# Kernel optimization log

Hardware: AMD Instinct MI355X
Metric: run time of the kernel (lower is better)

Reference implementation:

```python
import jax, jax.numpy as jnp
import numpy as np

N_NODES = 100000
N_EDGES = 1600000
IN_FEATS = 256
OUT_FEATS = 128


def setup_inputs() -> dict:
    key = jax.random.key(0)
    k1, k2, k3, k4, k5 = jax.random.split(key, 5)
    feat = jax.random.normal(k1, (N_NODES, IN_FEATS), dtype=jnp.float32)
    # xavier_uniform-like init for the weight
    limit = float(np.sqrt(6.0 / (IN_FEATS + OUT_FEATS)))
    weight = jax.random.uniform(k2, (IN_FEATS, OUT_FEATS), dtype=jnp.float32,
                                minval=-limit, maxval=limit)
    edge_weight = jax.random.uniform(k3, (N_EDGES,), dtype=jnp.float32)
    src = jax.random.randint(k4, (N_EDGES,), 0, N_NODES, dtype=jnp.int64)
    dst = jax.random.randint(k5, (N_EDGES,), 0, N_NODES, dtype=jnp.int64)
    return {"feat": feat, "weight": weight, "edge_weight": edge_weight,
            "src": src, "dst": dst}


def reference(feat, weight, edge_weight, src, dst):
    N = feat.shape[0]
    ones = jnp.ones(src.shape, dtype=feat.dtype)
    # out/in degrees from edge list (clamped to >= 1), as in DGL
    out_deg = jnp.clip(jax.ops.segment_sum(ones, src, num_segments=N), 1.0)
    in_deg = jnp.clip(jax.ops.segment_sum(ones, dst, num_segments=N), 1.0)
    # norm == 'both': pre-scale sources by out_deg^-0.5
    feat_src = feat * (out_deg ** -0.5)[:, None]
    # in_feats > out_feats branch: transform (with tanh) BEFORE aggregation
    h = jnp.tanh(feat_src @ weight)                      # [N, out]
    # message = u_mul_e: h[src] * edge_weight, then sum per destination
    m = h[src] * edge_weight[:, None]                    # [E, out]
    rst = jax.ops.segment_sum(m, dst, num_segments=N)    # [N, out]
    # norm == 'both': post-scale by in_deg^-0.5
    rst = rst * (in_deg ** -0.5)[:, None]
    return rst
```

## Files before the change

kernel.cpp:

```cpp
#include <hip/hip_runtime.h>
#include <hip/hip_fp16.h>
#include <math.h>

#define N_NODES 100000
#define N_EDGES 1600000
#define IN_F 256
#define OUT_F 128
#define SCAN_TPB 256
#define SCAN_EPB 1024

#define HR 4
#define HRANGE 25000
#define HC 64
#define HCHUNK 25000
#define PWORDS (N_NODES / 2)

typedef _Float16 h8 __attribute__((ext_vector_type(8)));
typedef float f4 __attribute__((ext_vector_type(4)));

__global__ __launch_bounds__(256) void hist_kernel(
        const int* __restrict__ src, const int* __restrict__ dst,
        int* __restrict__ rank, unsigned int* __restrict__ partial_in,
        unsigned int* __restrict__ partial_out) {
    __shared__ unsigned int bins[HRANGE / 2];
    int b = blockIdx.x;
    int c = b >> 3;
    int tr = b & 7;
    int type = tr >> 2;
    int r = tr & 3;
    for (int i = threadIdx.x; i < HRANGE / 2; i += 256) bins[i] = 0;
    __syncthreads();
    const int* nodes = type ? src : dst;
    const int e0 = c * HCHUNK;
    const int lo = r * HRANGE;
    const int ngroups = HCHUNK / 4;
    for (int g = threadIdx.x; g < ngroups; g += 256) {
        int e = e0 + g * 4;
        int4 n4 = *(const int4*)(nodes + e);
        int nn[4] = {n4.x, n4.y, n4.z, n4.w};
        #pragma unroll
        for (int j = 0; j < 4; ++j) {
            unsigned loc = (unsigned)(nn[j] - lo);
            if (loc < (unsigned)HRANGE) {
                unsigned sh = (loc & 1) * 16;
                unsigned old = atomicAdd(&bins[loc >> 1], 1u << sh);
                if (type == 0) rank[e + j] = (int)((old >> sh) & 0xffffu);
            }
        }
    }
    __syncthreads();
    unsigned int* part = type ? partial_out : partial_in;
    unsigned int* dstp = part + (size_t)c * PWORDS + (lo >> 1);
    for (int i = threadIdx.x; i < HRANGE / 2; i += 256) dstp[i] = bins[i];
}

__global__ __launch_bounds__(256) void fused_reduce_kernel(
        const unsigned int* __restrict__ partial_in,
        const unsigned int* __restrict__ partial_out,
        unsigned short* __restrict__ chunk_base16,
        int* __restrict__ deg_in, float* __restrict__ rs_out,
        int* __restrict__ spart, int N) {
    __shared__ int tmp[256];
    int t = threadIdx.x;
    int n0 = blockIdx.x * SCAN_EPB + t * 4;
    int run[4] = {0, 0, 0, 0};
    int sout[4] = {0, 0, 0, 0};
    if (n0 < N) {
        const int w0 = n0 >> 1;
        #pragma unroll 4
        for (int c = 0; c < HC; ++c) {
            ushort4 cb;
            cb.x = (unsigned short)run[0]; cb.y = (unsigned short)run[1];
            cb.z = (unsigned short)run[2]; cb.w = (unsigned short)run[3];
            *(ushort4*)(chunk_base16 + (size_t)c * N_NODES + n0) = cb;
            uint2 pi = *(const uint2*)(partial_in + (size_t)c * PWORDS + w0);
            run[0] += (int)(pi.x & 0xffffu);  run[1] += (int)(pi.x >> 16);
            run[2] += (int)(pi.y & 0xffffu);  run[3] += (int)(pi.y >> 16);
            uint2 po = *(const uint2*)(partial_out + (size_t)c * PWORDS + w0);
            sout[0] += (int)(po.x & 0xffffu); sout[1] += (int)(po.x >> 16);
            sout[2] += (int)(po.y & 0xffffu); sout[3] += (int)(po.y >> 16);
        }
        *(int4*)(deg_in + n0) = make_int4(run[0], run[1], run[2], run[3]);
        float4 rs;
        rs.x = rsqrtf((float)(sout[0] < 1 ? 1 : sout[0]));
        rs.y = rsqrtf((float)(sout[1] < 1 ? 1 : sout[1]));
        rs.z = rsqrtf((float)(sout[2] < 1 ? 1 : sout[2]));
        rs.w = rsqrtf((float)(sout[3] < 1 ? 1 : sout[3]));
        *(float4*)(rs_out + n0) = rs;
    }
    tmp[t] = run[0] + run[1] + run[2] + run[3];
    __syncthreads();
    for (int off = 128; off > 0; off >>= 1) {
        if (t < off) tmp[t] += tmp[t + off];
        __syncthreads();
    }
    if (t == 0) spart[blockIdx.x] = tmp[0];
}

__global__ __launch_bounds__(128) void scan_part2(const int* __restrict__ partials,
                                                  int* __restrict__ bases, int nb) {
    __shared__ int tmp[128];
    int t = threadIdx.x;
    int v = (t < nb) ? partials[t] : 0;
    tmp[t] = v;
    __syncthreads();
    int x = v;
    for (int off = 1; off < 128; off <<= 1) {
        int y = (t >= off) ? tmp[t - off] : 0;
        __syncthreads();
        x += y;
        tmp[t] = x;
        __syncthreads();
    }
    if (t < nb) bases[t] = x - v;
}

__global__ __launch_bounds__(SCAN_TPB) void scan_part3(const int* __restrict__ deg,
                                                       const int* __restrict__ bases,
                                                       int* __restrict__ row_ptr, int N) {
    __shared__ int tmp[SCAN_TPB];
    int t = threadIdx.x;
    int i0 = blockIdx.x * SCAN_EPB + t * 4;
    int v[4];
    int s = 0;
    #pragma unroll
    for (int j = 0; j < 4; ++j) { v[j] = (i0 + j < N) ? deg[i0 + j] : 0; s += v[j]; }
    tmp[t] = s;
    __syncthreads();
    int x = s;
    for (int off = 1; off < SCAN_TPB; off <<= 1) {
        int y = (t >= off) ? tmp[t - off] : 0;
        __syncthreads();
        x += y;
        tmp[t] = x;
        __syncthreads();
    }
    int excl = bases[blockIdx.x] + x - s;
    #pragma unroll
    for (int j = 0; j < 4; ++j) {
        if (i0 + j < N) row_ptr[i0 + j] = excl;
        excl += v[j];
    }
    if (blockIdx.x == gridDim.x - 1 && t == SCAN_TPB - 1) row_ptr[N] = bases[blockIdx.x] + x;
}

__global__ __launch_bounds__(256) void fill_kernel(
        const int* __restrict__ src, const int* __restrict__ dst,
        const float* __restrict__ ew, const int* __restrict__ row_ptr,
        const unsigned short* __restrict__ chunk_base16,
        const int* __restrict__ rank, int2* __restrict__ ed, int E) {
    int e0 = (blockIdx.x * 256 + threadIdx.x) * 4;
    if (e0 >= E) return;
    int4 s4 = *(const int4*)(src + e0);
    int4 d4 = *(const int4*)(dst + e0);
    float4 w4 = *(const float4*)(ew + e0);
    int4 r4 = *(const int4*)(rank + e0);
    int c = e0 / HCHUNK;
    const unsigned short* cb = chunk_base16 + (size_t)c * N_NODES;
    int dd[4] = {d4.x, d4.y, d4.z, d4.w};
    int ss[4] = {s4.x, s4.y, s4.z, s4.w};
    int rr[4] = {r4.x, r4.y, r4.z, r4.w};
    float ww[4] = {w4.x, w4.y, w4.z, w4.w};
    #pragma unroll
    for (int j = 0; j < 4; ++j) {
        int d = dd[j];
        int p = row_ptr[d] + (int)cb[d] + rr[j];
        unsigned long long v = (unsigned long long)(unsigned int)ss[j] |
                               ((unsigned long long)(unsigned int)__float_as_int(ww[j]) << 32);
        __builtin_nontemporal_store(v, (unsigned long long*)&ed[p]);
    }
}

__global__ void wt_kernel(const float* __restrict__ W, _Float16* __restrict__ Wt) {
    int i = blockIdx.x * blockDim.x + threadIdx.x;
    if (i < IN_F * OUT_F) {
        int n = i >> 8;
        int k = i & 255;
        Wt[i] = (_Float16)W[k * OUT_F + n];
    }
}

__global__ __launch_bounds__(256) void gemm_mfma_kernel(
        const float* __restrict__ feat, const _Float16* __restrict__ Wt,
        const float* __restrict__ rs_out, __half* __restrict__ h, int N) {
    const int wave = threadIdx.x >> 6;
    const int lane = threadIdx.x & 63;
    const int m = lane & 15;
    const int quad = lane >> 4;
    const int rowbase = blockIdx.x * 64 + wave * 16;
    const int arow = rowbase + m;
    const bool rowok = arow < N;

    const float rs = rowok ? rs_out[arow] : 1.f;
    const float* ap = feat + (size_t)(rowok ? arow : 0) * IN_F + quad * 8;

    f4 acc[8];
    #pragma unroll
    for (int t = 0; t < 8; ++t) acc[t] = (f4){0.f, 0.f, 0.f, 0.f};

    #pragma unroll
    for (int k0 = 0; k0 < IN_F; k0 += 32) {
        float4 f0 = make_float4(0.f, 0.f, 0.f, 0.f);
        float4 f1 = make_float4(0.f, 0.f, 0.f, 0.f);
        if (rowok) {
            f0 = *(const float4*)(ap + k0);
            f1 = *(const float4*)(ap + k0 + 4);
        }
        h8 a;
        a[0] = (_Float16)(f0.x * rs); a[1] = (_Float16)(f0.y * rs);
        a[2] = (_Float16)(f0.z * rs); a[3] = (_Float16)(f0.w * rs);
        a[4] = (_Float16)(f1.x * rs); a[5] = (_Float16)(f1.y * rs);
        a[6] = (_Float16)(f1.z * rs); a[7] = (_Float16)(f1.w * rs);
        const int k = k0 + quad * 8;
        #pragma unroll
        for (int t = 0; t < 8; ++t) {
            h8 b = *(const h8*)&Wt[(size_t)(t * 16 + m) * IN_F + k];
            acc[t] = __builtin_amdgcn_mfma_f32_16x16x32_f16(a, b, acc[t], 0, 0, 0);
        }
    }

    const int crow0 = rowbase + quad * 4;
    #pragma unroll
    for (int t = 0; t < 8; ++t) {
        #pragma unroll
        for (int r = 0; r < 4; ++r) {
            int rr = crow0 + r;
            if (rr < N) h[(size_t)rr * OUT_F + t * 16 + m] = __float2half(tanhf(acc[t][r]));
        }
    }
}

__global__ __launch_bounds__(256) void gather_kernel(
        const __half* __restrict__ h, const int2* __restrict__ ed,
        const int* __restrict__ row_ptr, float* __restrict__ out, int N) {
    int wave = threadIdx.x >> 6;
    int lane = threadIdx.x & 63;
    int node = blockIdx.x * 4 + wave;
    if (node >= N) return;
    int lo = row_ptr[node];
    int hi = row_ptr[node + 1];
    int p = lane >> 4;
    int c = lane & 15;
    float acc[4][8];
    #pragma unroll
    for (int g = 0; g < 4; ++g)
        #pragma unroll
        for (int i = 0; i < 8; ++i) acc[g][i] = 0.f;

    for (int j = lo; j < hi; j += 16) {
        #pragma unroll
        for (int g = 0; g < 4; ++g) {
            int jj = j + g * 4 + p;
            int2 e = (jj < hi) ? ed[jj] : make_int2(0, 0);
            float w = __int_as_float(e.y);
            int4 rrow = *(const int4*)(h + (size_t)e.x * OUT_F + c * 8);
            float2 t;
            t = __half22float2(*(__half2*)&rrow.x); acc[g][0] += w * t.x; acc[g][1] += w * t.y;
            t = __half22float2(*(__half2*)&rrow.y); acc[g][2] += w * t.x; acc[g][3] += w * t.y;
            t = __half22float2(*(__half2*)&rrow.z); acc[g][4] += w * t.x; acc[g][5] += w * t.y;
            t = __half22float2(*(__half2*)&rrow.w); acc[g][6] += w * t.x; acc[g][7] += w * t.y;
        }
    }
    float v[8];
    #pragma unroll
    for (int i = 0; i < 8; ++i) {
        v[i] = (acc[0][i] + acc[1][i]) + (acc[2][i] + acc[3][i]);
        v[i] += __shfl_xor(v[i], 16);
        v[i] += __shfl_xor(v[i], 32);
    }
    if (p == 0) {
        int deg = hi - lo; if (deg < 1) deg = 1;
        float rs = rsqrtf((float)deg);
        float* op = out + (size_t)node * OUT_F + c * 8;
        *(float4*)op       = make_float4(v[0] * rs, v[1] * rs, v[2] * rs, v[3] * rs);
        *(float4*)(op + 4) = make_float4(v[4] * rs, v[5] * rs, v[6] * rs, v[7] * rs);
    }
}

extern "C" void kernel_launch(void* const* d_in, const int* in_sizes, int n_in,
                              void* d_out, int out_size, void* d_ws, size_t ws_size,
                              hipStream_t stream) {
    const float* feat   = (const float*)d_in[0];
    const float* weight = (const float*)d_in[1];
    const float* ew     = (const float*)d_in[2];
    const int*   src    = (const int*)d_in[3];
    const int*   dst    = (const int*)d_in[4];
    float* out = (float*)d_out;

    char* ws = (char*)d_ws;
    float* rs_out      = (float*)(ws);
    int*   deg_in      = (int*)(ws + 400000);
    int*   row_ptr     = (int*)(ws + 800000);
    int*   spart       = (int*)(ws + 1200016);
    int*   sbases      = (int*)(ws + 1200528);
    int*   rank        = (int*)(ws + 1201056);
    unsigned int* partial_in  = (unsigned int*)(ws + 7601056);
    int2*  ed          = (int2*)(ws + 7601056);
    unsigned short* chunk_base16 = (unsigned short*)(ws + 20401056);
    unsigned int* partial_out = (unsigned int*)(ws + 33201056);
    __half* h          = (__half*)(ws + 20401056);
    _Float16* Wt       = (_Float16*)(ws + 46001056);

    const int nb = (N_NODES + SCAN_EPB - 1) / SCAN_EPB;

    hist_kernel<<<2 * HR * HC, 256, 0, stream>>>(src, dst, rank, partial_in, partial_out);
    fused_reduce_kernel<<<nb, 256, 0, stream>>>(partial_in, partial_out, chunk_base16,
                                                deg_in, rs_out, spart, N_NODES);
    scan_part2<<<1, 128, 0, stream>>>(spart, sbases, nb);
    scan_part3<<<nb, SCAN_TPB, 0, stream>>>(deg_in, sbases, row_ptr, N_NODES);
    fill_kernel<<<(N_EDGES / 4 + 255) / 256, 256, 0, stream>>>(src, dst, ew, row_ptr,
                                                               chunk_base16, rank, ed, N_EDGES);
    wt_kernel<<<(IN_F * OUT_F + 255) / 256, 256, 0, stream>>>(weight, Wt);
    gemm_mfma_kernel<<<(N_NODES + 63) / 64, 256, 0, stream>>>(feat, Wt, rs_out, h, N_NODES);
    gather_kernel<<<(N_NODES + 3) / 4, 256, 0, stream>>>(h, ed, row_ptr, out, N_NODES);
}
```

Measured before the change: 412.9 us.

## Split GEMM by output columns per wave and keep weight fragments in registers

Each wave now owns 32 output columns and keeps its weight B-fragments in registers for the whole block. It loops over the block's 64 rows in pairs of 16-row tiles, rather than each wave owning 16 rows and reloading all of W for every k-step. The out-degree row scale moves from the fp32→fp16 input conversion to the accumulator epilogue, so each feature element needs one fewer multiply. The cost is that all four waves in a block now read the same feat rows, which leans on cache for reuse, and register pressure rises from holding 16 h8 B fragments.

Result: faster. 403.0 us (-2.4%).

```diff
diff --git a/kernel.cpp b/kernel.cpp
--- a/kernel.cpp
+++ b/kernel.cpp
@@ -187,45 +187,63 @@
     const int lane = threadIdx.x & 63;
     const int m = lane & 15;
     const int quad = lane >> 4;
-    const int rowbase = blockIdx.x * 64 + wave * 16;
-    const int arow = rowbase + m;
-    const bool rowok = arow < N;
-
-    const float rs = rowok ? rs_out[arow] : 1.f;
-    const float* ap = feat + (size_t)(rowok ? arow : 0) * IN_F + quad * 8;
-
-    f4 acc[8];
-    #pragma unroll
-    for (int t = 0; t < 8; ++t) acc[t] = (f4){0.f, 0.f, 0.f, 0.f};
-
-    #pragma unroll
-    for (int k0 = 0; k0 < IN_F; k0 += 32) {
-        float4 f0 = make_float4(0.f, 0.f, 0.f, 0.f);
-        float4 f1 = make_float4(0.f, 0.f, 0.f, 0.f);
-        if (rowok) {
-            f0 = *(const float4*)(ap + k0);
-            f1 = *(const float4*)(ap + k0 + 4);
-        }
-        h8 a;
-        a[0] = (_Float16)(f0.x * rs); a[1] = (_Float16)(f0.y * rs);
-        a[2] = (_Float16)(f0.z * rs); a[3] = (_Float16)(f0.w * rs);
-        a[4] = (_Float16)(f1.x * rs); a[5] = (_Float16)(f1.y * rs);
-        a[6] = (_Float16)(f1.z * rs); a[7] = (_Float16)(f1.w * rs);
-        const int k = k0 + quad * 8;
-        #pragma unroll
-        for (int t = 0; t < 8; ++t) {
-            h8 b = *(const h8*)&Wt[(size_t)(t * 16 + m) * IN_F + k];
-            acc[t] = __builtin_amdgcn_mfma_f32_16x16x32_f16(a, b, acc[t], 0, 0, 0);
-        }
-    }
-
-    const int crow0 = rowbase + quad * 4;
-    #pragma unroll
-    for (int t = 0; t < 8; ++t) {
-        #pragma unroll
-        for (int r = 0; r < 4; ++r) {
-            int rr = crow0 + r;
-            if (rr < N) h[(size_t)rr * OUT_F + t * 16 + m] = __float2half(tanhf(acc[t][r]));
+    const int n0 = wave * 32;
+
+    h8 b[2][8];
+    #pragma unroll
+    for (int t = 0; t < 2; ++t)
+        #pragma unroll
+        for (int k = 0; k < 8; ++k)
+            b[t][k] = *(const h8*)&Wt[(size_t)(n0 + t * 16 + m) * IN_F + k * 32 + quad * 8];
+
+    const int rowbase = blockIdx.x * 64;
+
+    #pragma unroll
+    for (int pair = 0; pair < 2; ++pair) {
+        const int r0 = rowbase + pair * 32;
+        int ar0 = r0 + m;       if (ar0 >= N) ar0 = 0;
+        int ar1 = r0 + 16 + m;  if (ar1 >= N) ar1 = 0;
+        const float* ap0 = feat + (size_t)ar0 * IN_F + quad * 8;
+        const float* ap1 = feat + (size_t)ar1 * IN_F + quad * 8;
+
+        f4 acc00 = {0.f, 0.f, 0.f, 0.f}, acc01 = {0.f, 0.f, 0.f, 0.f};
+        f4 acc10 = {0.f, 0.f, 0.f, 0.f}, acc11 = {0.f, 0.f, 0.f, 0.f};
+
+        #pragma unroll
+        for (int k = 0; k < 8; ++k) {
+            float4 f00 = *(const float4*)(ap0 + k * 32);
+            float4 f01 = *(const float4*)(ap0 + k * 32 + 4);
+            float4 f10 = *(const float4*)(ap1 + k * 32);
+            float4 f11 = *(const float4*)(ap1 + k * 32 + 4);
+            h8 a0, a1;
+            a0[0] = (_Float16)f00.x; a0[1] = (_Float16)f00.y;
+            a0[2] = (_Float16)f00.z; a0[3] = (_Float16)f00.w;
+            a0[4] = (_Float16)f01.x; a0[5] = (_Float16)f01.y;
+            a0[6] = (_Float16)f01.z; a0[7] = (_Float16)f01.w;
+            a1[0] = (_Float16)f10.x; a1[1] = (_Float16)f10.y;
+            a1[2] = (_Float16)f10.z; a1[3] = (_Float16)f10.w;
+            a1[4] = (_Float16)f11.x; a1[5] = (_Float16)f11.y;
+            a1[6] = (_Float16)f11.z; a1[7] = (_Float16)f11.w;
+            acc00 = __builtin_amdgcn_mfma_f32_16x16x32_f16(a0, b[0][k], acc00, 0, 0, 0);
+            acc01 = __builtin_amdgcn_mfma_f32_16x16x32_f16(a0, b[1][k], acc01, 0, 0, 0);
+            acc10 = __builtin_amdgcn_mfma_f32_16x16x32_f16(a1, b[0][k], acc10, 0, 0, 0);
+            acc11 = __builtin_amdgcn_mfma_f32_16x16x32_f16(a1, b[1][k], acc11, 0, 0, 0);
+        }
+
+        #pragma unroll
+        for (int tile = 0; tile < 2; ++tile) {
+            const f4 aL = tile ? acc10 : acc00;
+            const f4 aR = tile ? acc11 : acc01;
+            const int crow = r0 + tile * 16 + quad * 4;
+            #pragma unroll
+            for (int r = 0; r < 4; ++r) {
+                const int rr = crow + r;
+                if (rr < N) {
+                    const float rs = rs_out[rr];
+                    h[(size_t)rr * OUT_F + n0 + m]      = __float2half(tanhf(aL[r] * rs));
+                    h[(size_t)rr * OUT_F + n0 + 16 + m] = __float2half(tanhf(aR[r] * rs));
+                }
+            }
         }
     }
 }
```

## Stage GEMM tiles through double-buffered LDS with async global-to-LDS loads

Applied to the files above, without the earlier changes.

The GEMM kernel is restructured to stage feature and weight tiles into double-buffered shared memory using global_load_lds, with an XOR swizzle on the A tile and a new wave-to-output-column mapping. The next K-tile is prefetched while MFMAs run on the current one. The row scaling by rs_out moves from the input to the epilogue, and tanhf is replaced by an exp-based fast tanh. This aims to hide the latency of the feature loads and reuse the weight tile across waves, at the cost of LDS usage, block barriers, and slightly different rounding in the tanh and the fp16 cast.

After: 377.2 us. 8.6% less time.

```diff
diff --git a/kernel.cpp b/kernel.cpp
--- a/kernel.cpp
+++ b/kernel.cpp
@@ -15,8 +15,15 @@
 #define HCHUNK 25000
 #define PWORDS (N_NODES / 2)
 
+#define GM_ROWS 64
+#define BK 32
+
 typedef _Float16 h8 __attribute__((ext_vector_type(8)));
 typedef float f4 __attribute__((ext_vector_type(4)));
+
+#define GLD16(gp, lp) __builtin_amdgcn_global_load_lds( \
+    (const __attribute__((address_space(1))) unsigned int*)(gp), \
+    (__attribute__((address_space(3))) unsigned int*)(lp), 16, 0, 0)
 
 __global__ __launch_bounds__(256) void hist_kernel(
         const int* __restrict__ src, const int* __restrict__ dst,
@@ -180,52 +187,91 @@
     }
 }
 
-__global__ __launch_bounds__(256) void gemm_mfma_kernel(
+__device__ __forceinline__ float fast_tanh(float x) {
+    float e = __expf(2.0f * x);
+    return 1.0f - 2.0f / (e + 1.0f);
+}
+
+__global__ __launch_bounds__(256, 4) void gemm_mfma_kernel(
         const float* __restrict__ feat, const _Float16* __restrict__ Wt,
         const float* __restrict__ rs_out, __half* __restrict__ h, int N) {
-    const int wave = threadIdx.x >> 6;
-    const int lane = threadIdx.x & 63;
-    const int m = lane & 15;
+    __shared__ float    a_lds[2][GM_ROWS * BK];
+    __shared__ _Float16 b_lds[2][OUT_F * BK];
+
+    const int tid  = threadIdx.x;
+    const int wave = tid >> 6;
+    const int lane = tid & 63;
+    const int m    = lane & 15;
     const int quad = lane >> 4;
-    const int rowbase = blockIdx.x * 64 + wave * 16;
-    const int arow = rowbase + m;
-    const bool rowok = arow < N;
-
-    const float rs = rowok ? rs_out[arow] : 1.f;
-    const float* ap = feat + (size_t)(rowok ? arow : 0) * IN_F + quad * 8;
-
-    f4 acc[8];
-    #pragma unroll
-    for (int t = 0; t < 8; ++t) acc[t] = (f4){0.f, 0.f, 0.f, 0.f};
-
-    #pragma unroll
-    for (int k0 = 0; k0 < IN_F; k0 += 32) {
-        float4 f0 = make_float4(0.f, 0.f, 0.f, 0.f);
-        float4 f1 = make_float4(0.f, 0.f, 0.f, 0.f);
-        if (rowok) {
-            f0 = *(const float4*)(ap + k0);
-            f1 = *(const float4*)(ap + k0 + 4);
-        }
-        h8 a;
-        a[0] = (_Float16)(f0.x * rs); a[1] = (_Float16)(f0.y * rs);
-        a[2] = (_Float16)(f0.z * rs); a[3] = (_Float16)(f0.w * rs);
-        a[4] = (_Float16)(f1.x * rs); a[5] = (_Float16)(f1.y * rs);
-        a[6] = (_Float16)(f1.z * rs); a[7] = (_Float16)(f1.w * rs);
-        const int k = k0 + quad * 8;
-        #pragma unroll
-        for (int t = 0; t < 8; ++t) {
-            h8 b = *(const h8*)&Wt[(size_t)(t * 16 + m) * IN_F + k];
-            acc[t] = __builtin_amdgcn_mfma_f32_16x16x32_f16(a, b, acc[t], 0, 0, 0);
-        }
-    }
-
-    const int crow0 = rowbase + quad * 4;
-    #pragma unroll
-    for (int t = 0; t < 8; ++t) {
+    const int n0   = wave * 32;
+    const int r0   = blockIdx.x * GM_ROWS;
+
+    const int l3 = lane >> 3;
+    const int ag = (lane & 7) ^ l3;
+    int arow0 = r0 + 16 * wave + l3;      if (arow0 >= N) arow0 = N - 1;
+    int arow1 = r0 + 16 * wave + 8 + l3;  if (arow1 >= N) arow1 = N - 1;
+    const float* ga0 = feat + (size_t)arow0 * IN_F + ag * 4;
+    const float* ga1 = feat + (size_t)arow1 * IN_F + ag * 4;
+    const int brow0 = 32 * wave + (lane >> 2);
+    const int brow1 = 32 * wave + 16 + (lane >> 2);
+    const _Float16* gb0 = Wt + (size_t)brow0 * IN_F + (lane & 3) * 8;
+    const _Float16* gb1 = Wt + (size_t)brow1 * IN_F + (lane & 3) * 8;
+
+    f4 acc[4][2];
+    #pragma unroll
+    for (int t = 0; t < 4; ++t) {
+        acc[t][0] = (f4){0.f, 0.f, 0.f, 0.f};
+        acc[t][1] = (f4){0.f, 0.f, 0.f, 0.f};
+    }
+
+    GLD16(ga0, &a_lds[0][(16 * wave) * BK]);
+    GLD16(ga1, &a_lds[0][(16 * wave + 8) * BK]);
+    GLD16(gb0, &b_lds[0][(32 * wave) * BK]);
+    GLD16(gb1, &b_lds[0][(32 * wave + 16) * BK]);
+    __syncthreads();
+
+    #pragma unroll
+    for (int kt = 0; kt < IN_F / BK; ++kt) {
+        const int cb = kt & 1;
+        if (kt < IN_F / BK - 1) {
+            const int nb2 = cb ^ 1;
+            const int ko = (kt + 1) * BK;
+            GLD16(ga0 + ko, &a_lds[nb2][(16 * wave) * BK]);
+            GLD16(ga1 + ko, &a_lds[nb2][(16 * wave + 8) * BK]);
+            GLD16(gb0 + ko, &b_lds[nb2][(32 * wave) * BK]);
+            GLD16(gb1 + ko, &b_lds[nb2][(32 * wave + 16) * BK]);
+            __builtin_amdgcn_sched_barrier(0);
+        }
+        h8 b0 = *(const h8*)&b_lds[cb][(n0 + m) * BK + quad * 8];
+        h8 b1 = *(const h8*)&b_lds[cb][(n0 + 16 + m) * BK + quad * 8];
+        #pragma unroll
+        for (int t = 0; t < 4; ++t) {
+            const int ar = t * 16 + m;
+            float4 alo = *(const float4*)&a_lds[cb][ar * BK + (((quad * 2)     ^ (m & 7)) * 4)];
+            float4 ahi = *(const float4*)&a_lds[cb][ar * BK + (((quad * 2 + 1) ^ (m & 7)) * 4)];
+            h8 a;
+            a[0] = (_Float16)alo.x; a[1] = (_Float16)alo.y;
+            a[2] = (_Float16)alo.z; a[3] = (_Float16)alo.w;
+            a[4] = (_Float16)ahi.x; a[5] = (_Float16)ahi.y;
+            a[6] = (_Float16)ahi.z; a[7] = (_Float16)ahi.w;
+            acc[t][0] = __builtin_amdgcn_mfma_f32_16x16x32_f16(a, b0, acc[t][0], 0, 0, 0);
+            acc[t][1] = __builtin_amdgcn_mfma_f32_16x16x32_f16(a, b1, acc[t][1], 0, 0, 0);
+        }
+        __syncthreads();
+    }
+
+    #pragma unroll
+    for (int t = 0; t < 4; ++t) {
+        const int crow = r0 + t * 16 + quad * 4;
+        float4 rs4 = *(const float4*)&rs_out[crow];
+        const float rsv[4] = {rs4.x, rs4.y, rs4.z, rs4.w};
         #pragma unroll
         for (int r = 0; r < 4; ++r) {
-            int rr = crow0 + r;
-            if (rr < N) h[(size_t)rr * OUT_F + t * 16 + m] = __float2half(tanhf(acc[t][r]));
+            const int rr = crow + r;
+            if (rr < N) {
+                h[(size_t)rr * OUT_F + n0 + m]      = __float2half(fast_tanh(acc[t][0][r] * rsv[r]));
+                h[(size_t)rr * OUT_F + n0 + 16 + m] = __float2half(fast_tanh(acc[t][1][r] * rsv[r]));
+            }
         }
     }
 }
@@ -311,6 +357,6 @@
     fill_kernel<<<(N_EDGES / 4 + 255) / 256, 256, 0, stream>>>(src, dst, ew, row_ptr,
                                                                chunk_base16, rank, ed, N_EDGES);
     wt_kernel<<<(IN_F * OUT_F + 255) / 256, 256, 0, stream>>>(weight, Wt);
-    gemm_mfma_kernel<<<(N_NODES + 63) / 64, 256, 0, stream>>>(feat, Wt, rs_out, h, N_NODES);
+    gemm_mfma_kernel<<<(N_NODES + GM_ROWS - 1) / GM_ROWS, 256, 0, stream>>>(feat, Wt, rs_out, h, N_NODES);
     gather_kernel<<<(N_NODES + 3) / 4, 256, 0, stream>>>(h, ed, row_ptr, out, N_NODES);
 }
```
